# Kernel optimization log

Hardware: AMD Instinct MI355X
Metric: run time of the kernel (lower is better)

Reference implementation:

```python
import jax, jax.numpy as jnp
import numpy as np

L_CHUNK = 5   # frames per camera chunk (hardcoded L=5 in similarity())
N_CAMS = 6    # len(cam_list)
TOP_K = 8     # hardcoded K=8 in similarity()
HEADS = 8


def setup_inputs() -> dict:
    key = jax.random.key(0)
    ks = jax.random.split(key, 5)
    B, M, N, C = 1, L_CHUNK * N_CAMS, 261, 2048  # M = S*P = 30 multiview token groups
    scale = 0.02
    tokens = jax.random.normal(ks[0], (B, M, N, C), dtype=jnp.float32)
    Wq = jax.random.normal(ks[1], (C, C), dtype=jnp.float32) * scale
    Wk = jax.random.normal(ks[2], (C, C), dtype=jnp.float32) * scale
    Wv = jax.random.normal(ks[3], (C, C), dtype=jnp.float32) * scale
    Wo = jax.random.normal(ks[4], (C, C), dtype=jnp.float32) * scale
    return {"tokens": tokens, "Wq": Wq, "Wk": Wk, "Wv": Wv, "Wo": Wo}


def _similarity(pose_tokens):
    # pose_tokens: [B, M, C] -> block-diag-biased softmax sim + topk neighbors
    sim = jnp.einsum('bmc,bnc->bmn', pose_tokens, pose_tokens)
    block = jnp.kron(jnp.eye(N_CAMS, dtype=sim.dtype),
                     jnp.ones((L_CHUNK, L_CHUNK), dtype=sim.dtype))  # [M, M]
    sim = sim + 10000.0 * block
    probs = jax.nn.softmax(sim, axis=-1)
    vals, idx = jax.lax.top_k(probs, TOP_K)  # [B, M, K]
    return vals, idx


def reference(tokens, Wq, Wk, Wv, Wo):
    B, M, N, C = tokens.shape
    H = HEADS
    d = C // H
    # similarity + topk over camera/pose tokens (token index 0 of each group)
    vals, idx = _similarity(tokens[:, :, 0, :])
    # gather K neighbor token groups per (batch, group): [B, M, K, N, C]
    nbr = jax.vmap(lambda t, i: t[i])(tokens, idx)
    nbr = nbr.reshape(B, M, TOP_K * N, C)
    q = (tokens @ Wq).reshape(B, M, N, H, d)
    k = (nbr @ Wk).reshape(B, M, TOP_K * N, H, d)
    v = (nbr @ Wv).reshape(B, M, TOP_K * N, H, d)
    scores = jnp.einsum('bmqhd,bmkhd->bmhqk', q, k) / jnp.sqrt(jnp.asarray(d, q.dtype))
    # weight each neighbor's tokens by its topk similarity value (log-bias)
    bias = jnp.repeat(jnp.log(vals + 1e-6), N, axis=-1)  # [B, M, K*N]
    scores = scores + bias[:, :, None, None, :]
    attn = jax.nn.softmax(scores, axis=-1)
    out = jnp.einsum('bmhqk,bmkhd->bmqhd', attn, v).reshape(B, M, N, C)
    return tokens + out @ Wo
```

## Files before the change

### kernel.cpp

```cpp
#include <hip/hip_runtime.h>
#include <stdint.h>

#define MTOK 7830
#define MPAD 7936
#define CD   2048
#define VTC  7920
#define AS1 __attribute__((address_space(1)))
#define AS3 __attribute__((address_space(3)))

typedef unsigned short u16;
typedef __bf16 bf16x8 __attribute__((ext_vector_type(8)));
typedef float f32x4 __attribute__((ext_vector_type(4)));
typedef unsigned short u16x8 __attribute__((ext_vector_type(8)));

__device__ __forceinline__ u16 f2bf(float f) {
  unsigned x = __float_as_uint(f);
  return (u16)((x + 0x7fffu + ((x >> 16) & 1u)) >> 16);
}

__device__ __forceinline__ void gld16(const u16* g, u16* l) {
  __builtin_amdgcn_global_load_lds((AS1 const unsigned int*)(g), (AS3 unsigned int*)(l), 16, 0, 0);
}

__global__ void cvt_tokens(const float* __restrict__ T, u16* __restrict__ O) {
  int row = blockIdx.x;
  size_t base = (size_t)row * CD + threadIdx.x * 8;
  u16x8 o = {0,0,0,0,0,0,0,0};
  if (row < MTOK) {
    const float* s = T + base;
    #pragma unroll
    for (int j = 0; j < 8; ++j) o[j] = f2bf(s[j]);
  }
  *(u16x8*)&O[base] = o;
}

__global__ void cvt_w(const float* __restrict__ Wq, const float* __restrict__ Wk,
                      const float* __restrict__ Wv, const float* __restrict__ Wo,
                      u16* __restrict__ WqkvT, u16* __restrict__ WoT) {
  __shared__ float tile[32][33];
  int k0 = blockIdx.x * 32;
  int n0 = blockIdx.y * 32;
  const float* W; u16* Dst; int nl0, dr0;
  if (n0 < 2048)      { W = Wq; Dst = WqkvT; nl0 = n0;        dr0 = n0; }
  else if (n0 < 4096) { W = Wk; Dst = WqkvT; nl0 = n0 - 2048; dr0 = n0; }
  else if (n0 < 6144) { W = Wv; Dst = WqkvT; nl0 = n0 - 4096; dr0 = n0; }
  else                { W = Wo; Dst = WoT;   nl0 = n0 - 6144; dr0 = n0 - 6144; }
  int tx = threadIdx.x, ty = threadIdx.y;
  #pragma unroll
  for (int i = 0; i < 4; ++i)
    tile[ty + i*8][tx] = W[(size_t)(k0 + ty + i*8) * CD + nl0 + tx];
  __syncthreads();
  #pragma unroll
  for (int i = 0; i < 4; ++i) {
    int n = ty + i*8;
    Dst[(size_t)(dr0 + n) * CD + k0 + tx] = f2bf(tile[tx][n]);
  }
}

__global__ void posesim(const float* __restrict__ tok, float* __restrict__ sim) {
  int mm = blockIdx.y, nn = blockIdx.x;
  if (nn < mm) return;
  const float* a = tok + (size_t)mm * 261 * CD;
  const float* b = tok + (size_t)nn * 261 * CD;
  int tid = threadIdx.x;
  float p = 0.f;
  for (int j = tid; j < CD; j += 256) p += a[j] * b[j];
  __shared__ float red[256];
  red[tid] = p; __syncthreads();
  for (int s = 128; s > 0; s >>= 1) { if (tid < s) red[tid] += red[tid + s]; __syncthreads(); }
  if (tid == 0) {
    float v = red[0];
    float bb = ((mm/5) == (nn/5)) ? 10000.0f : 0.0f;
    sim[mm*30 + nn] = v + bb;
    if (nn != mm) sim[nn*30 + mm] = v + bb;
  }
}

__global__ void topk_bias(const float* __restrict__ sim, float* __restrict__ bias,
                          int* __restrict__ idxo) {
  int m = threadIdx.x;
  if (m >= 30) return;
  float p[30];
  float mx = -1e30f;
  for (int j = 0; j < 30; ++j) { p[j] = sim[m*30 + j]; mx = fmaxf(mx, p[j]); }
  float z = 0.f;
  for (int j = 0; j < 30; ++j) { p[j] = __expf(p[j] - mx); z += p[j]; }
  float inv = 1.0f / z;
  for (int j = 0; j < 30; ++j) p[j] *= inv;
  for (int k = 0; k < 8; ++k) {
    int bj = 0; float bv = p[0];
    for (int j = 1; j < 30; ++j) if (p[j] > bv) { bv = p[j]; bj = j; }
    idxo[m*8 + k] = bj;
    bias[m*8 + k] = logf(bv + 1e-6f);
    p[bj] = -1.0f;
  }
}

template<int EPI>
__global__ __launch_bounds__(512) void gemm_bt(
    const u16* __restrict__ A, const u16* __restrict__ Bt,
    u16* __restrict__ Cq, u16* __restrict__ Cv,
    const float* __restrict__ resid, float* __restrict__ Dout, int K)
{
  __shared__ u16 Al[2][256 * 64];
  __shared__ u16 Bl[2][256 * 64];
  int tid = threadIdx.x, lane = tid & 63, wid = tid >> 6;
  int lo4 = lane & 15, hi2 = lane >> 4;
  int lin = blockIdx.y * gridDim.x + blockIdx.x;
  int q8  = (gridDim.x * gridDim.y) >> 3;
  int lin2 = (lin & 7) * q8 + (lin >> 3);
  int bn = lin2 % gridDim.x, bm = lin2 / gridDim.x;
  int wy = wid >> 2, wx = wid & 3;
  int r8 = lane >> 3, c8 = lane & 7;

  f32x4 acc[8][4] = {};

  size_t aofs[4], bofs[4];
  #pragma unroll
  for (int j = 0; j < 4; ++j) {
    int row = wid*32 + j*8 + r8;
    int sw = 8 * (c8 ^ (row & 7));
    aofs[j] = (size_t)(bm*256 + row) * K + sw;
    bofs[j] = (size_t)(bn*256 + row) * K + sw;
  }
  int ldst = wid * 2048;

  int nK = K >> 6;
  #pragma unroll
  for (int j = 0; j < 4; ++j) {
    gld16(A  + aofs[j], &Al[0][ldst + j*512]);
    gld16(Bt + bofs[j], &Bl[0][ldst + j*512]);
  }
  #pragma unroll
  for (int j = 0; j < 4; ++j) {
    gld16(A  + 64 + aofs[j], &Al[1][ldst + j*512]);
    gld16(Bt + 64 + bofs[j], &Bl[1][ldst + j*512]);
  }

  for (int t = 0; t < nK; ++t) {
    if (t + 1 < nK) asm volatile("s_waitcnt vmcnt(8)" ::: "memory");
    else            asm volatile("s_waitcnt vmcnt(0)" ::: "memory");
    __builtin_amdgcn_sched_barrier(0);
    __builtin_amdgcn_s_barrier();
    __builtin_amdgcn_sched_barrier(0);

    const u16* Ac = Al[t & 1];
    const u16* Bc = Bl[t & 1];

    bf16x8 bv[4][2];
    #pragma unroll
    for (int ni = 0; ni < 4; ++ni) {
      int br = wx*64 + ni*16 + lo4;
      #pragma unroll
      for (int kk = 0; kk < 2; ++kk)
        bv[ni][kk] = *(const bf16x8*)&Bc[br*64 + 8*((kk*4 + hi2) ^ (br & 7))];
    }

    #pragma unroll
    for (int mg = 0; mg < 2; ++mg) {
      bf16x8 av[4][2];
      #pragma unroll
      for (int mi = 0; mi < 4; ++mi) {
        int ar = wy*128 + mg*64 + mi*16 + lo4;
        #pragma unroll
        for (int kk = 0; kk < 2; ++kk)
          av[mi][kk] = *(const bf16x8*)&Ac[ar*64 + 8*((kk*4 + hi2) ^ (ar & 7))];
      }
      __builtin_amdgcn_s_setprio(1);
      #pragma unroll
      for (int kk = 0; kk < 2; ++kk)
        #pragma unroll
        for (int mi = 0; mi < 4; ++mi)
          #pragma unroll
          for (int ni = 0; ni < 4; ++ni)
            acc[mg*4 + mi][ni] = __builtin_amdgcn_mfma_f32_16x16x32_bf16(
                av[mi][kk], bv[ni][kk], acc[mg*4 + mi][ni], 0, 0, 0);
      __builtin_amdgcn_s_setprio(0);
      if (mg == 0) {
        __builtin_amdgcn_s_barrier();
      } else {
        __builtin_amdgcn_sched_barrier(0);
        if (t + 2 < nK) {
          size_t kn = (size_t)(t + 2) << 6;
          u16* An = Al[t & 1];
          u16* Bn = Bl[t & 1];
          #pragma unroll
          for (int j = 0; j < 4; ++j) {
            gld16(A  + kn + aofs[j], &An[ldst + j*512]);
            gld16(Bt + kn + bofs[j], &Bn[ldst + j*512]);
          }
        }
        __builtin_amdgcn_sched_barrier(0);
      }
    }
  }

  int gm0 = bm*256 + wy*128;
  int gn0 = bn*256 + wx*64;
  #pragma unroll
  for (int mi = 0; mi < 8; ++mi) {
    #pragma unroll
    for (int ni = 0; ni < 4; ++ni) {
      int gmb = gm0 + mi*16 + hi2*4;
      int gn  = gn0 + ni*16 + lo4;
      #pragma unroll
      for (int r = 0; r < 4; ++r) {
        float v = acc[mi][ni][r];
        int gm = gmb + r;
        if (EPI == 0) {
          if (gn < 4096) {
            Cq[(size_t)gm * 4096 + gn] = f2bf(v);
          } else if (gm < MTOK) {
            int g = gm / 261, tk = gm - g * 261;
            Cv[(size_t)(gn - 4096) * VTC + g * 264 + tk] = f2bf(v);
          }
        } else {
          if (gm < MTOK) {
            size_t off = (size_t)gm * CD + gn;
            Dout[off] = resid[off] + v;
          }
        }
      }
    }
  }
}

__global__ __launch_bounds__(512) void attn_main(
    const u16* __restrict__ QK,
    const u16* __restrict__ VtG,
    const float* __restrict__ bias, const int* __restrict__ idx,
    u16* __restrict__ AO)
{
  int h = blockIdx.x, m = blockIdx.y;
  int tid = threadIdx.x, lane = tid & 63, wid = tid >> 6;
  int lo4 = lane & 15, hi2 = lane >> 4;

  __shared__ u16 Kl[2][32 * 256];
  __shared__ u16 Vl[2][256 * 32];
  __shared__ u16 Pl[8][2][16 * 50];
  __shared__ float bias_s[8];
  __shared__ int   idx_s[8];
  if (tid < 8) {
    bias_s[tid] = bias[m*8 + tid] * 1.4426950408889634f;
    idx_s[tid]  = idx[m*8 + tid];
  }

  bf16x8 qf[2][8];
  #pragma unroll
  for (int qg = 0; qg < 2; ++qg) {
    int qrow = m*261 + wid*32 + qg*16 + lo4;
    #pragma unroll
    for (int kk = 0; kk < 8; ++kk)
      qf[qg][kk] = *(const bf16x8*)&QK[(size_t)qrow * 4096 + h*256 + kk*32 + hi2*8];
  }

  size_t kofs[2], vofs[2];
  #pragma unroll
  for (int i = 0; i < 2; ++i) {
    int rt = 4*wid + 2*i + (lane >> 5);
    kofs[i] = (size_t)rt * 4096 + 2048 + h*256 + 8*((lane & 31) ^ (rt & 7));
    int vdr = 32*wid + 16*i + (lane >> 2);
    vofs[i] = (size_t)(h*256 + vdr) * VTC + 8*((lane & 3) ^ ((vdr >> 1) & 3));
  }
  int ld0 = wid * 1024;

  f32x4 O[2][16] = {};
  float srun[2][4] = {};
  const float SC = 0.09016844f;

  {
    int ig0 = idx[m*8];
    #pragma unroll
    for (int i = 0; i < 2; ++i) {
      gld16(QK + (size_t)(ig0*261) * 4096 + kofs[i], &Kl[0][ld0 + i*512]);
      gld16(VtG + (size_t)(ig0*264) + vofs[i],       &Vl[0][ld0 + i*512]);
    }
  }

  int vswz = 8 * (hi2 ^ ((lo4 >> 1) & 3));
  int kxb  = (lo4 >> 2) & 1;
  int kswz = 8 * (hi2 ^ (lo4 & 3));

  for (int it = 0; it < 72; ++it) {
    __syncthreads();
    if (it + 1 < 72) {
      int tn = it + 1;
      int gg = tn / 9;
      int tok0n = (tn - gg*9) * 32;
      int ign = idx_s[gg];
      #pragma unroll
      for (int i = 0; i < 2; ++i) {
        gld16(QK + (size_t)(ign*261 + tok0n) * 4096 + kofs[i], &Kl[tn & 1][ld0 + i*512]);
        gld16(VtG + (size_t)(ign*264 + tok0n) + vofs[i],       &Vl[tn & 1][ld0 + i*512]);
      }
    }
    {
      int gg = it / 9;
      int tok0 = (it - gg*9) * 32;
      float bgl = bias_s[gg];
      const u16* Kb = Kl[it & 1];
      const u16* Vb = Vl[it & 1];

      f32x4 sv[2][2] = {};
      __builtin_amdgcn_s_setprio(1);
      #pragma unroll
      for (int kk = 0; kk < 8; ++kk) {
        int off = lo4*256 + 32*(kk ^ kxb) + kswz;
        bf16x8 kb0 = *(const bf16x8*)&Kb[off];
        bf16x8 kb1 = *(const bf16x8*)&Kb[off + 16*256];
        sv[0][0] = __builtin_amdgcn_mfma_f32_16x16x32_bf16(qf[0][kk], kb0, sv[0][0], 0, 0, 0);
        sv[0][1] = __builtin_amdgcn_mfma_f32_16x16x32_bf16(qf[0][kk], kb1, sv[0][1], 0, 0, 0);
        sv[1][0] = __builtin_amdgcn_mfma_f32_16x16x32_bf16(qf[1][kk], kb0, sv[1][0], 0, 0, 0);
        sv[1][1] = __builtin_amdgcn_mfma_f32_16x16x32_bf16(qf[1][kk], kb1, sv[1][1], 0, 0, 0);
      }
      __builtin_amdgcn_s_setprio(0);
      bool v0 = (tok0 + lo4) < 261, v1 = (tok0 + 16 + lo4) < 261;
      #pragma unroll
      for (int qg = 0; qg < 2; ++qg) {
        u16* Pw = Pl[wid][qg];
        #pragma unroll
        for (int r = 0; r < 4; ++r) {
          float e0 = __builtin_exp2f(fmaf(sv[qg][0][r], SC, bgl));
          float e1 = __builtin_exp2f(fmaf(sv[qg][1][r], SC, bgl));
          e0 = v0 ? e0 : 0.f;
          e1 = v1 ? e1 : 0.f;
          srun[qg][r] += e0 + e1;
          Pw[(hi2*4 + r)*50 + lo4]      = f2bf(e0);
          Pw[(hi2*4 + r)*50 + 16 + lo4] = f2bf(e1);
        }
      }
      bf16x8 pa0 = *(const bf16x8*)&Pl[wid][0][lo4*50 + hi2*8];
      bf16x8 pa1 = *(const bf16x8*)&Pl[wid][1][lo4*50 + hi2*8];
      __builtin_amdgcn_s_setprio(1);
      #pragma unroll
      for (int o = 0; o < 16; ++o) {
        bf16x8 vv = *(const bf16x8*)&Vb[(o*16 + lo4)*32 + vswz];
        O[0][o] = __builtin_amdgcn_mfma_f32_16x16x32_bf16(pa0, vv, O[0][o], 0, 0, 0);
        O[1][o] = __builtin_amdgcn_mfma_f32_16x16x32_bf16(pa1, vv, O[1][o], 0, 0, 0);
      }
      __builtin_amdgcn_s_setprio(0);
    }
  }

  #pragma unroll
  for (int qg = 0; qg < 2; ++qg) {
    float inv[4];
    #pragma unroll
    for (int r = 0; r < 4; ++r) {
      float s = srun[qg][r];
      s += __shfl_xor(s, 1);
      s += __shfl_xor(s, 2);
      s += __shfl_xor(s, 4);
      s += __shfl_xor(s, 8);
      inv[r] = 1.0f / s;
    }
    #pragma unroll
    for (int o = 0; o < 16; ++o) {
      #pragma unroll
      for (int r = 0; r < 4; ++r) {
        int qq = wid*32 + qg*16 + hi2*4 + r;
        AO[(size_t)(m*261 + qq) * CD + h*256 + o*16 + lo4] = f2bf(O[qg][o][r] * inv[r]);
      }
    }
  }
}

__global__ __launch_bounds__(512) void attn_tail(
    const u16* __restrict__ QK, const u16* __restrict__ VtG,
    const float* __restrict__ bias, const int* __restrict__ idx,
    u16* __restrict__ AO)
{
  int h = blockIdx.x, m = blockIdx.y;
  int tid = threadIdx.x, lane = tid & 63, wid = tid >> 6;
  int lo4 = lane & 15, hi2 = lane >> 4;

  __shared__ float Om[8][16][256];
  __shared__ float Sm[8][16];
  __shared__ u16 Pl[8][16 * 50];

  int q = 256 + lo4;
  bool qv = q < 261;
  int qrow = m*261 + (qv ? q : 0);
  bf16x8 qf[8];
  #pragma unroll
  for (int kk = 0; kk < 8; ++kk) {
    u16x8 u = {0,0,0,0,0,0,0,0};
    if (qv) u = *(const u16x8*)&QK[(size_t)qrow * 4096 + h*256 + kk*32 + hi2*8];
    qf[kk] = __builtin_bit_cast(bf16x8, u);
  }

  f32x4 O[16] = {};
  float srun[4] = {0.f, 0.f, 0.f, 0.f};
  const float SC = 0.09016844f;

  for (int it = wid; it < 72; it += 8) {
    int gg = it / 9;
    int tok0 = (it - gg*9) * 32;
    int ig = idx[m*8 + gg];
    float bgl = bias[m*8 + gg] * 1.4426950408889634f;
    const u16* kbase = QK + (size_t)(ig*261 + tok0) * 4096 + 2048 + h*256;
    f32x4 s0v = {0,0,0,0}, s1v = {0,0,0,0};
    #pragma unroll
    for (int kk = 0; kk < 8; ++kk) {
      bf16x8 kb0 = *(const bf16x8*)&kbase[(size_t)lo4 * 4096 + kk*32 + hi2*8];
      bf16x8 kb1 = *(const bf16x8*)&kbase[(size_t)(16 + lo4) * 4096 + kk*32 + hi2*8];
      s0v = __builtin_amdgcn_mfma_f32_16x16x32_bf16(qf[kk], kb0, s0v, 0, 0, 0);
      s1v = __builtin_amdgcn_mfma_f32_16x16x32_bf16(qf[kk], kb1, s1v, 0, 0, 0);
    }
    bool v0 = (tok0 + lo4) < 261, v1 = (tok0 + 16 + lo4) < 261;
    float p0[4], p1[4];
    #pragma unroll
    for (int r = 0; r < 4; ++r) {
      float e0 = __builtin_exp2f(fmaf(s0v[r], SC, bgl));
      float e1 = __builtin_exp2f(fmaf(s1v[r], SC, bgl));
      e0 = v0 ? e0 : 0.f;
      e1 = v1 ? e1 : 0.f;
      srun[r] += e0 + e1;
      p0[r] = e0; p1[r] = e1;
    }
    u16* Pw = Pl[wid];
    #pragma unroll
    for (int r = 0; r < 4; ++r) {
      Pw[(hi2*4 + r)*50 + lo4]      = f2bf(p0[r]);
      Pw[(hi2*4 + r)*50 + 16 + lo4] = f2bf(p1[r]);
    }
    bf16x8 pa = *(const bf16x8*)&Pw[lo4*50 + hi2*8];
    const u16* vbase = VtG + (size_t)(h*256) * VTC + ig*264 + tok0;
    #pragma unroll
    for (int o = 0; o < 16; ++o) {
      bf16x8 vv = *(const bf16x8*)&vbase[(size_t)(o*16 + lo4) * VTC + hi2*8];
      O[o] = __builtin_amdgcn_mfma_f32_16x16x32_bf16(pa, vv, O[o], 0, 0, 0);
    }
  }

  #pragma unroll
  for (int r = 0; r < 4; ++r) {
    float s = srun[r];
    s += __shfl_xor(s, 1);
    s += __shfl_xor(s, 2);
    s += __shfl_xor(s, 4);
    s += __shfl_xor(s, 8);
    srun[r] = s;
  }
  #pragma unroll
  for (int o = 0; o < 16; ++o)
    #pragma unroll
    for (int r = 0; r < 4; ++r)
      Om[wid][hi2*4 + r][o*16 + lo4] = O[o][r];
  if (lo4 == 0) {
    #pragma unroll
    for (int r = 0; r < 4; ++r) Sm[wid][hi2*4 + r] = srun[r];
  }
  __syncthreads();
  if (wid == 0) {
    #pragma unroll
    for (int o = 0; o < 16; ++o) {
      #pragma unroll
      for (int r = 0; r < 4; ++r) {
        int row = hi2*4 + r;
        int qq = 256 + row;
        if (qq < 261) {
          int c = o*16 + lo4;
          float v = 0.f, s = 0.f;
          #pragma unroll
          for (int w = 0; w < 8; ++w) { v += Om[w][row][c]; s += Sm[w][row]; }
          AO[(size_t)(m*261 + qq) * CD + h*256 + c] = f2bf(v / s);
        }
      }
    }
  }
}

extern "C" void kernel_launch(void* const* d_in, const int* in_sizes, int n_in,
                              void* d_out, int out_size, void* d_ws, size_t ws_size,
                              hipStream_t stream) {
  const float* tokens = (const float*)d_in[0];
  const float* Wq = (const float*)d_in[1];
  const float* Wk = (const float*)d_in[2];
  const float* Wv = (const float*)d_in[3];
  const float* Wo = (const float*)d_in[4];
  float* out = (float*)d_out;
  char* ws = (char*)d_ws;

  constexpr size_t OFF_TOKBF = 0;
  constexpr size_t OFF_WQKVT = OFF_TOKBF + (size_t)MPAD * CD * 2;
  constexpr size_t OFF_WOT   = OFF_WQKVT + (size_t)6144 * CD * 2;
  constexpr size_t OFF_QK    = OFF_WOT   + (size_t)CD * CD * 2;
  constexpr size_t OFF_VTG   = OFF_QK    + (size_t)MPAD * 4096 * 2;
  constexpr size_t OFF_AO    = OFF_VTG   + (size_t)CD * VTC * 2 + 4096;
  constexpr size_t OFF_SIM   = OFF_AO    + (size_t)MPAD * CD * 2;
  constexpr size_t OFF_BIAS  = OFF_SIM   + 4096;
  constexpr size_t OFF_IDX   = OFF_BIAS  + 1024;

  u16* tokBf  = (u16*)(ws + OFF_TOKBF);
  u16* WqkvT  = (u16*)(ws + OFF_WQKVT);
  u16* WoT    = (u16*)(ws + OFF_WOT);
  u16* QKbuf  = (u16*)(ws + OFF_QK);
  u16* VtG    = (u16*)(ws + OFF_VTG);
  u16* attnO  = (u16*)(ws + OFF_AO);
  float* simw = (float*)(ws + OFF_SIM);
  float* bw   = (float*)(ws + OFF_BIAS);
  int*   iw   = (int*)(ws + OFF_IDX);

  cvt_tokens<<<MPAD, 256, 0, stream>>>(tokens, tokBf);
  cvt_w<<<dim3(64, 256), dim3(32, 8), 0, stream>>>(Wq, Wk, Wv, Wo, WqkvT, WoT);
  posesim<<<dim3(30, 30), 256, 0, stream>>>(tokens, simw);
  topk_bias<<<1, 32, 0, stream>>>(simw, bw, iw);
  gemm_bt<0><<<dim3(24, 31), 512, 0, stream>>>(tokBf, WqkvT, QKbuf, VtG, nullptr, nullptr, CD);
  attn_tail<<<dim3(8, 30), 512, 0, stream>>>(QKbuf, VtG, bw, iw, attnO);
  attn_main<<<dim3(8, 30), 512, 0, stream>>>(QKbuf, VtG, bw, iw, attnO);
  gemm_bt<1><<<dim3(8, 31), 512, 0, stream>>>(attnO, WoT, nullptr, nullptr, tokens, out, CD);
}
```

Measured before the change: 644.0 us.

## Restructure GEMM main loop into 4-stage K=32 pipeline with interleaved loads

The bf16 GEMM now uses four LDS stages of 32-wide K slices instead of two 64-wide stages, keeping three slices in flight and using a matching 4-column XOR swizzle. Global-to-LDS loads for the stage three ahead are split into two halves and issued between the two MFMA groups of each iteration. The goal is deeper prefetch and finer interleaving of memory traffic with MFMA work to hide load latency. In exchange there are twice as many loop iterations and barriers per K, and a narrower swizzle that may cause more LDS bank conflicts.

```diff
diff --git a/kernel.cpp b/kernel.cpp
--- a/kernel.cpp
+++ b/kernel.cpp
@@ -102,8 +102,8 @@
     u16* __restrict__ Cq, u16* __restrict__ Cv,
     const float* __restrict__ resid, float* __restrict__ Dout, int K)
 {
-  __shared__ u16 Al[2][256 * 64];
-  __shared__ u16 Bl[2][256 * 64];
+  __shared__ u16 Al[4][256 * 32];
+  __shared__ u16 Bl[4][256 * 32];
   int tid = threadIdx.x, lane = tid & 63, wid = tid >> 6;
   int lo4 = lane & 15, hi2 = lane >> 4;
   int lin = blockIdx.y * gridDim.x + blockIdx.x;
@@ -111,88 +111,90 @@
   int lin2 = (lin & 7) * q8 + (lin >> 3);
   int bn = lin2 % gridDim.x, bm = lin2 / gridDim.x;
   int wy = wid >> 2, wx = wid & 3;
-  int r8 = lane >> 3, c8 = lane & 7;
+  int r4 = lane >> 2, c4 = lane & 3;
 
   f32x4 acc[8][4] = {};
 
-  size_t aofs[4], bofs[4];
-  #pragma unroll
-  for (int j = 0; j < 4; ++j) {
-    int row = wid*32 + j*8 + r8;
-    int sw = 8 * (c8 ^ (row & 7));
-    aofs[j] = (size_t)(bm*256 + row) * K + sw;
-    bofs[j] = (size_t)(bn*256 + row) * K + sw;
-  }
-  int ldst = wid * 2048;
-
-  int nK = K >> 6;
-  #pragma unroll
-  for (int j = 0; j < 4; ++j) {
-    gld16(A  + aofs[j], &Al[0][ldst + j*512]);
-    gld16(Bt + bofs[j], &Bl[0][ldst + j*512]);
-  }
-  #pragma unroll
-  for (int j = 0; j < 4; ++j) {
-    gld16(A  + 64 + aofs[j], &Al[1][ldst + j*512]);
-    gld16(Bt + 64 + bofs[j], &Bl[1][ldst + j*512]);
-  }
-
-  for (int t = 0; t < nK; ++t) {
-    if (t + 1 < nK) asm volatile("s_waitcnt vmcnt(8)" ::: "memory");
-    else            asm volatile("s_waitcnt vmcnt(0)" ::: "memory");
+  size_t aoc[2], boc[2];
+  #pragma unroll
+  for (int ci = 0; ci < 2; ++ci) {
+    int rt = wid*32 + ci*16 + r4;
+    int gs = 8 * (c4 ^ (rt & 3));
+    aoc[ci] = (size_t)(bm*256 + rt) * K + gs;
+    boc[ci] = (size_t)(bn*256 + rt) * K + gs;
+  }
+  int ldw = wid * 1024;
+
+  int nH = (K >> 5);
+  #pragma unroll
+  for (int Hs = 0; Hs < 3; ++Hs) {
+    size_t kh = (size_t)(Hs >> 1) * 64 + (Hs & 1) * 32;
+    #pragma unroll
+    for (int ci = 0; ci < 2; ++ci) {
+      gld16(A  + kh + aoc[ci], &Al[Hs][ldw + ci*512]);
+      gld16(Bt + kh + boc[ci], &Bl[Hs][ldw + ci*512]);
+    }
+  }
+
+  for (int H = 0; H < nH; ++H) {
+    if (H + 2 < nH)      asm volatile("s_waitcnt vmcnt(8)" ::: "memory");
+    else if (H + 1 < nH) asm volatile("s_waitcnt vmcnt(4)" ::: "memory");
+    else                 asm volatile("s_waitcnt vmcnt(0)" ::: "memory");
     __builtin_amdgcn_sched_barrier(0);
     __builtin_amdgcn_s_barrier();
     __builtin_amdgcn_sched_barrier(0);
 
-    const u16* Ac = Al[t & 1];
-    const u16* Bc = Bl[t & 1];
-
-    bf16x8 bv[4][2];
+    const u16* Ac = Al[H & 3];
+    const u16* Bc = Bl[H & 3];
+    bool st = (H + 3) < nH;
+    int Hs = H + 3;
+    size_t kh = (size_t)(Hs >> 1) * 64 + (Hs & 1) * 32;
+    u16* An = Al[Hs & 3];
+    u16* Bn = Bl[Hs & 3];
+
+    bf16x8 bv[4], av[4];
     #pragma unroll
     for (int ni = 0; ni < 4; ++ni) {
       int br = wx*64 + ni*16 + lo4;
-      #pragma unroll
-      for (int kk = 0; kk < 2; ++kk)
-        bv[ni][kk] = *(const bf16x8*)&Bc[br*64 + 8*((kk*4 + hi2) ^ (br & 7))];
-    }
-
-    #pragma unroll
-    for (int mg = 0; mg < 2; ++mg) {
-      bf16x8 av[4][2];
-      #pragma unroll
-      for (int mi = 0; mi < 4; ++mi) {
-        int ar = wy*128 + mg*64 + mi*16 + lo4;
-        #pragma unroll
-        for (int kk = 0; kk < 2; ++kk)
-          av[mi][kk] = *(const bf16x8*)&Ac[ar*64 + 8*((kk*4 + hi2) ^ (ar & 7))];
-      }
-      __builtin_amdgcn_s_setprio(1);
-      #pragma unroll
-      for (int kk = 0; kk < 2; ++kk)
-        #pragma unroll
-        for (int mi = 0; mi < 4; ++mi)
-          #pragma unroll
-          for (int ni = 0; ni < 4; ++ni)
-            acc[mg*4 + mi][ni] = __builtin_amdgcn_mfma_f32_16x16x32_bf16(
-                av[mi][kk], bv[ni][kk], acc[mg*4 + mi][ni], 0, 0, 0);
-      __builtin_amdgcn_s_setprio(0);
-      if (mg == 0) {
-        __builtin_amdgcn_s_barrier();
-      } else {
-        __builtin_amdgcn_sched_barrier(0);
-        if (t + 2 < nK) {
-          size_t kn = (size_t)(t + 2) << 6;
-          u16* An = Al[t & 1];
-          u16* Bn = Bl[t & 1];
-          #pragma unroll
-          for (int j = 0; j < 4; ++j) {
-            gld16(A  + kn + aofs[j], &An[ldst + j*512]);
-            gld16(Bt + kn + bofs[j], &Bn[ldst + j*512]);
-          }
-        }
-        __builtin_amdgcn_sched_barrier(0);
-      }
-    }
+      bv[ni] = *(const bf16x8*)&Bc[br*32 + 8*(hi2 ^ (br & 3))];
+    }
+    #pragma unroll
+    for (int mi = 0; mi < 4; ++mi) {
+      int ar = wy*128 + mi*16 + lo4;
+      av[mi] = *(const bf16x8*)&Ac[ar*32 + 8*(hi2 ^ (ar & 3))];
+    }
+    if (st) {
+      gld16(A  + kh + aoc[0], &An[ldw]);
+      gld16(Bt + kh + boc[0], &Bn[ldw]);
+    }
+    __builtin_amdgcn_sched_barrier(0);
+    __builtin_amdgcn_s_barrier();
+    __builtin_amdgcn_s_setprio(1);
+    #pragma unroll
+    for (int mi = 0; mi < 4; ++mi)
+      #pragma unroll
+      for (int ni = 0; ni < 4; ++ni)
+        acc[mi][ni] = __builtin_amdgcn_mfma_f32_16x16x32_bf16(av[mi], bv[ni], acc[mi][ni], 0, 0, 0);
+    __builtin_amdgcn_s_setprio(0);
+
+    #pragma unroll
+    for (int mi = 0; mi < 4; ++mi) {
+      int ar = wy*128 + 64 + mi*16 + lo4;
+      av[mi] = *(const bf16x8*)&Ac[ar*32 + 8*(hi2 ^ (ar & 3))];
+    }
+    if (st) {
+      gld16(A  + kh + aoc[1], &An[ldw + 512]);
+      gld16(Bt + kh + boc[1], &Bn[ldw + 512]);
+    }
+    __builtin_amdgcn_sched_barrier(0);
+    __builtin_amdgcn_s_barrier();
+    __builtin_amdgcn_s_setprio(1);
+    #pragma unroll
+    for (int mi = 0; mi < 4; ++mi)
+      #pragma unroll
+      for (int ni = 0; ni < 4; ++ni)
+        acc[4 + mi][ni] = __builtin_amdgcn_mfma_f32_16x16x32_bf16(av[mi], bv[ni], acc[4 + mi][ni], 0, 0, 0);
+    __builtin_amdgcn_s_setprio(0);
   }
 
   int gm0 = bm*256 + wy*128;
```

Result: slower. 673.4 us (+4.6%).

## Fold attention tail rows into main kernel via a ninth wavefront

Applied to the files above, without the earlier changes.

Removes the separate attn_tail kernel, which handled the last 5 query rows of each group by splitting keys across waves and reducing through shared memory. attn_main is widened from 512 to 576 threads so a ninth wave handles query rows 256–287, with stores masked to rows below 261. The K/V tile loads are still issued only by the first eight waves. This saves one kernel launch and the tail's strided, uncached global K/V reads. The costs are that the ninth wave does full-tile work for only 5 valid rows, and the higher launch bound lowers the per-thread register budget, which could cause spills for the large accumulator arrays.

```diff
diff --git a/kernel.cpp b/kernel.cpp
--- a/kernel.cpp
+++ b/kernel.cpp
@@ -225,7 +225,7 @@
   }
 }
 
-__global__ __launch_bounds__(512) void attn_main(
+__global__ __launch_bounds__(576) void attn_main(
     const u16* __restrict__ QK,
     const u16* __restrict__ VtG,
     const float* __restrict__ bias, const int* __restrict__ idx,
@@ -237,7 +237,7 @@
 
   __shared__ u16 Kl[2][32 * 256];
   __shared__ u16 Vl[2][256 * 32];
-  __shared__ u16 Pl[8][2][16 * 50];
+  __shared__ u16 Pl[9][2][16 * 50];
   __shared__ float bias_s[8];
   __shared__ int   idx_s[8];
   if (tid < 8) {
@@ -268,7 +268,7 @@
   float srun[2][4] = {};
   const float SC = 0.09016844f;
 
-  {
+  if (wid < 8) {
     int ig0 = idx[m*8];
     #pragma unroll
     for (int i = 0; i < 2; ++i) {
@@ -283,7 +283,7 @@
 
   for (int it = 0; it < 72; ++it) {
     __syncthreads();
-    if (it + 1 < 72) {
+    if (it + 1 < 72 && wid < 8) {
       int tn = it + 1;
       int gg = tn / 9;
       int tok0n = (tn - gg*9) * 32;
@@ -359,113 +359,8 @@
       #pragma unroll
       for (int r = 0; r < 4; ++r) {
         int qq = wid*32 + qg*16 + hi2*4 + r;
-        AO[(size_t)(m*261 + qq) * CD + h*256 + o*16 + lo4] = f2bf(O[qg][o][r] * inv[r]);
-      }
-    }
-  }
-}
-
-__global__ __launch_bounds__(512) void attn_tail(
-    const u16* __restrict__ QK, const u16* __restrict__ VtG,
-    const float* __restrict__ bias, const int* __restrict__ idx,
-    u16* __restrict__ AO)
-{
-  int h = blockIdx.x, m = blockIdx.y;
-  int tid = threadIdx.x, lane = tid & 63, wid = tid >> 6;
-  int lo4 = lane & 15, hi2 = lane >> 4;
-
-  __shared__ float Om[8][16][256];
-  __shared__ float Sm[8][16];
-  __shared__ u16 Pl[8][16 * 50];
-
-  int q = 256 + lo4;
-  bool qv = q < 261;
-  int qrow = m*261 + (qv ? q : 0);
-  bf16x8 qf[8];
-  #pragma unroll
-  for (int kk = 0; kk < 8; ++kk) {
-    u16x8 u = {0,0,0,0,0,0,0,0};
-    if (qv) u = *(const u16x8*)&QK[(size_t)qrow * 4096 + h*256 + kk*32 + hi2*8];
-    qf[kk] = __builtin_bit_cast(bf16x8, u);
-  }
-
-  f32x4 O[16] = {};
-  float srun[4] = {0.f, 0.f, 0.f, 0.f};
-  const float SC = 0.09016844f;
-
-  for (int it = wid; it < 72; it += 8) {
-    int gg = it / 9;
-    int tok0 = (it - gg*9) * 32;
-    int ig = idx[m*8 + gg];
-    float bgl = bias[m*8 + gg] * 1.4426950408889634f;
-    const u16* kbase = QK + (size_t)(ig*261 + tok0) * 4096 + 2048 + h*256;
-    f32x4 s0v = {0,0,0,0}, s1v = {0,0,0,0};
-    #pragma unroll
-    for (int kk = 0; kk < 8; ++kk) {
-      bf16x8 kb0 = *(const bf16x8*)&kbase[(size_t)lo4 * 4096 + kk*32 + hi2*8];
-      bf16x8 kb1 = *(const bf16x8*)&kbase[(size_t)(16 + lo4) * 4096 + kk*32 + hi2*8];
-      s0v = __builtin_amdgcn_mfma_f32_16x16x32_bf16(qf[kk], kb0, s0v, 0, 0, 0);
-      s1v = __builtin_amdgcn_mfma_f32_16x16x32_bf16(qf[kk], kb1, s1v, 0, 0, 0);
-    }
-    bool v0 = (tok0 + lo4) < 261, v1 = (tok0 + 16 + lo4) < 261;
-    float p0[4], p1[4];
-    #pragma unroll
-    for (int r = 0; r < 4; ++r) {
-      float e0 = __builtin_exp2f(fmaf(s0v[r], SC, bgl));
-      float e1 = __builtin_exp2f(fmaf(s1v[r], SC, bgl));
-      e0 = v0 ? e0 : 0.f;
-      e1 = v1 ? e1 : 0.f;
-      srun[r] += e0 + e1;
-      p0[r] = e0; p1[r] = e1;
-    }
-    u16* Pw = Pl[wid];
-    #pragma unroll
-    for (int r = 0; r < 4; ++r) {
-      Pw[(hi2*4 + r)*50 + lo4]      = f2bf(p0[r]);
-      Pw[(hi2*4 + r)*50 + 16 + lo4] = f2bf(p1[r]);
-    }
-    bf16x8 pa = *(const bf16x8*)&Pw[lo4*50 + hi2*8];
-    const u16* vbase = VtG + (size_t)(h*256) * VTC + ig*264 + tok0;
-    #pragma unroll
-    for (int o = 0; o < 16; ++o) {
-      bf16x8 vv = *(const bf16x8*)&vbase[(size_t)(o*16 + lo4) * VTC + hi2*8];
-      O[o] = __builtin_amdgcn_mfma_f32_16x16x32_bf16(pa, vv, O[o], 0, 0, 0);
-    }
-  }
-
-  #pragma unroll
-  for (int r = 0; r < 4; ++r) {
-    float s = srun[r];
-    s += __shfl_xor(s, 1);
-    s += __shfl_xor(s, 2);
-    s += __shfl_xor(s, 4);
-    s += __shfl_xor(s, 8);
-    srun[r] = s;
-  }
-  #pragma unroll
-  for (int o = 0; o < 16; ++o)
-    #pragma unroll
-    for (int r = 0; r < 4; ++r)
-      Om[wid][hi2*4 + r][o*16 + lo4] = O[o][r];
-  if (lo4 == 0) {
-    #pragma unroll
-    for (int r = 0; r < 4; ++r) Sm[wid][hi2*4 + r] = srun[r];
-  }
-  __syncthreads();
-  if (wid == 0) {
-    #pragma unroll
-    for (int o = 0; o < 16; ++o) {
-      #pragma unroll
-      for (int r = 0; r < 4; ++r) {
-        int row = hi2*4 + r;
-        int qq = 256 + row;
-        if (qq < 261) {
-          int c = o*16 + lo4;
-          float v = 0.f, s = 0.f;
-          #pragma unroll
-          for (int w = 0; w < 8; ++w) { v += Om[w][row][c]; s += Sm[w][row]; }
-          AO[(size_t)(m*261 + qq) * CD + h*256 + c] = f2bf(v / s);
-        }
+        if (qq < 261)
+          AO[(size_t)(m*261 + qq) * CD + h*256 + o*16 + lo4] = f2bf(O[qg][o][r] * inv[r]);
       }
     }
   }
@@ -507,7 +402,6 @@
   posesim<<<dim3(30, 30), 256, 0, stream>>>(tokens, simw);
   topk_bias<<<1, 32, 0, stream>>>(simw, bw, iw);
   gemm_bt<0><<<dim3(24, 31), 512, 0, stream>>>(tokBf, WqkvT, QKbuf, VtG, nullptr, nullptr, CD);
-  attn_tail<<<dim3(8, 30), 512, 0, stream>>>(QKbuf, VtG, bw, iw, attnO);
-  attn_main<<<dim3(8, 30), 512, 0, stream>>>(QKbuf, VtG, bw, iw, attnO);
+  attn_main<<<dim3(8, 30), 576, 0, stream>>>(QKbuf, VtG, bw, iw, attnO);
   gemm_bt<1><<<dim3(8, 31), 512, 0, stream>>>(attnO, WoT, nullptr, nullptr, tokens, out, CD);
 }
```

After: 1.196 ms. +85.7%, slower.
